# Optimization experiments

Measured on AMD Instinct MI355X. Metric: run time of the kernel, lower is better.

The kernel has to match this reference:

```python
import jax, jax.numpy as jnp
import numpy as np


def _conv3x3(x, w, b):
    # standard 3x3 conv, stride 1, padding 1, NCHW/OIHW
    y = jax.lax.conv_general_dilated(
        x, w, window_strides=(1, 1), padding=((1, 1), (1, 1)),
        dimension_numbers=('NCHW', 'OIHW', 'NCHW'))
    return y + b[None, :, None, None]


def _deform_conv3x3(x, offset, w, b):
    # torchvision-style DeformConv2d: kernel 3x3, stride 1, pad 1, dilation 1,
    # 1 offset group, no mask. offset: [B, 18, H, W] with (dy, dx) per tap.
    B, C, H, W = x.shape
    K = 9
    off = offset.reshape(B, K, 2, H, W)
    ky = (jnp.arange(K) // 3 - 1).astype(x.dtype)[None, :, None, None]
    kx = (jnp.arange(K) % 3 - 1).astype(x.dtype)[None, :, None, None]
    # fractional sample positions per output pixel and kernel tap: [B, K, H, W]
    sy = off[:, :, 0] + ky + jnp.arange(H, dtype=x.dtype)[None, None, :, None]
    sx = off[:, :, 1] + kx + jnp.arange(W, dtype=x.dtype)[None, None, None, :]
    y0f = jnp.floor(sy)
    x0f = jnp.floor(sx)
    dy = sy - y0f
    dx = sx - x0f
    y0 = y0f.astype(jnp.int32)
    x0 = x0f.astype(jnp.int32)

    def sample_b(xb, yi, xi):
        # xb: [C,H,W], yi/xi: [K,H,W] -> [C,K,H,W], zero outside bounds
        valid = (yi >= 0) & (yi < H) & (xi >= 0) & (xi < W)
        yc = jnp.clip(yi, 0, H - 1)
        xc = jnp.clip(xi, 0, W - 1)
        return xb[:, yc, xc] * valid[None].astype(xb.dtype)

    def bilinear_b(xb, y0b, x0b, dyb, dxb):
        v00 = sample_b(xb, y0b, x0b)
        v01 = sample_b(xb, y0b, x0b + 1)
        v10 = sample_b(xb, y0b + 1, x0b)
        v11 = sample_b(xb, y0b + 1, x0b + 1)
        w00 = ((1 - dyb) * (1 - dxb))[None]
        w01 = ((1 - dyb) * dxb)[None]
        w10 = (dyb * (1 - dxb))[None]
        w11 = (dyb * dxb)[None]
        return v00 * w00 + v01 * w01 + v10 * w10 + v11 * w11

    samp = jax.vmap(bilinear_b)(x, y0, x0, dy, dx)  # [B, C, K, H, W]
    Co, Ci = w.shape[0], w.shape[1]
    out = jnp.einsum('oik,bikhw->bohw', w.reshape(Co, Ci, K), samp)
    return out + b[None, :, None, None]


def setup_inputs() -> dict:
    key = jax.random.key(0)
    ks = jax.random.split(key, 5)
    B, C, H, W = 4, 128, 96, 96
    lr = jax.random.normal(ks[0], (B, C, H, W), jnp.float32)
    hr = jax.random.normal(ks[1], (B, C, H, W), jnp.float32)
    w_off = jax.random.normal(ks[2], (18, 2 * C, 3, 3), jnp.float32) * 0.02
    b_off = jnp.zeros((18,), jnp.float32)
    w_def = jax.random.normal(ks[3], (C, C, 3, 3), jnp.float32) / np.float32(np.sqrt(C * 9))
    b_def = jax.random.normal(ks[4], (C,), jnp.float32) * 0.01
    return {"lr_features": lr, "hr_features": hr, "w_off": w_off,
            "b_off": b_off, "w_def": w_def, "b_def": b_def}


def reference(lr_features, hr_features, w_off, b_off, w_def, b_def):
    inp = jnp.concatenate([lr_features, hr_features], axis=1)  # [B, 2C, H, W]
    offset = _conv3x3(inp, w_off, b_off)                        # [B, 18, H, W]
    return _deform_conv3x3(hr_features, offset, w_def, b_def)   # [B, C, H, W]
```

## Files before the change

### kernel.cpp

```cpp
#include <hip/hip_runtime.h>
#include <hip/hip_bf16.h>

#define HH 96
#define WW 96
#define CC 128
#define C2 256
#define PLANE (HH*WW)
#define NGRP 6
#define GP 8
#define NG 16
#define KSG 72
#define ROWS 13
#define NPCHK (ROWS*WW)
#define PCHK_PAD 1280

typedef __attribute__((ext_vector_type(8))) short bf16x8;
typedef __attribute__((ext_vector_type(4))) float f32x4;
typedef __attribute__((ext_vector_type(4))) unsigned int u32x4;

__device__ __forceinline__ int swz(int row, int byte_in_row) {
    return row * 128 + (byte_in_row ^ ((row & 7) << 4));
}

__device__ __forceinline__ void gload_lds16(const void* g, void* l) {
    __builtin_amdgcn_global_load_lds(
        (const __attribute__((address_space(1))) char*)g,
        (__attribute__((address_space(3))) char*)l, 16, 0, 0);
}

__device__ __forceinline__ unsigned pack2(float a, float b) {
    return (unsigned)__bfloat16_as_ushort(__float2bfloat16(a)) |
           ((unsigned)__bfloat16_as_ushort(__float2bfloat16(b)) << 16);
}

#define MFMA16(A,B,C) __builtin_amdgcn_mfma_f32_16x16x32_bf16((A),(B),(C),0,0,0)

#define VMW4() { asm volatile("s_waitcnt vmcnt(4)" ::: "memory"); __builtin_amdgcn_sched_barrier(0); }
#define VMW0() { asm volatile("s_waitcnt vmcnt(0)" ::: "memory"); __builtin_amdgcn_sched_barrier(0); }
#define LGKM0_BAR() { asm volatile("s_waitcnt lgkmcnt(0)" ::: "memory"); \
    __builtin_amdgcn_sched_barrier(0); __builtin_amdgcn_s_barrier(); \
    __builtin_amdgcn_sched_barrier(0); }
#define RAW_BAR() { __builtin_amdgcn_sched_barrier(0); __builtin_amdgcn_s_barrier(); \
    __builtin_amdgcn_sched_barrier(0); }

__global__ __launch_bounds__(256) void prep_kernel(
    const float* __restrict__ hr, const float* __restrict__ lr,
    const float* __restrict__ w_def, const float* __restrict__ w_off,
    unsigned short* __restrict__ hrbf, unsigned short* __restrict__ lrbf,
    unsigned short* __restrict__ wpad, unsigned short* __restrict__ wop)
{
    const int bid = blockIdx.x;
    const int tid = threadIdx.x;
    if (bid < 4608) {
        const bool is_hr = bid < 2304;
        const float* src0 = is_hr ? hr : lr;
        unsigned short* o = is_hr ? hrbf : lrbf;
        int idx = (is_hr ? bid : bid - 2304) * 256 + tid;
        int hw = idx % PLANE;
        int t  = idx / PLANE;
        int g  = t & 15;
        int b  = t >> 4;
        const float* src = src0 + ((size_t)(b * CC + g * GP)) * PLANE + hw;
        unsigned pk[4];
#pragma unroll
        for (int j = 0; j < 4; ++j)
            pk[j] = pack2(src[(size_t)(2*j) * PLANE], src[(size_t)(2*j+1) * PLANE]);
        u32x4 v = {pk[0], pk[1], pk[2], pk[3]};
        *reinterpret_cast<u32x4*>(o + (size_t)idx * 8) = v;
    } else if (bid < 5184) {
        int i = (bid - 4608) * 256 + tid;
        int oc = i / (NG * KSG);
        int r  = i - oc * (NG * KSG);
        int g  = r / KSG;
        int s  = r - g * KSG;
        int tap = s >> 3;
        int icoff = s & 7;
        wpad[i] = __bfloat16_as_ushort(__float2bfloat16(
            w_def[(size_t)(oc * CC + g * GP + icoff) * 9 + tap]));
    } else {
        int i = (bid - 5184) * 256 + tid;
        int oc = i / (32 * KSG);
        int r  = i - oc * (32 * KSG);
        int g  = r / KSG;
        int s  = r - g * KSG;
        int tap = s >> 3;
        int icoff = s & 7;
        int c = g * 8 + icoff;
        float v = (oc < 18) ? w_off[(size_t)(oc * C2 + c) * 9 + tap] : 0.f;
        wop[i] = __bfloat16_as_ushort(__float2bfloat16(v));
    }
}

__global__ __launch_bounds__(256) void wcvt_kernel(const float* __restrict__ w,
                                                   unsigned short* __restrict__ o)
{
    int i = blockIdx.x * 256 + threadIdx.x;
    if (i < CC * NG * KSG) {
        int oc = i / (NG * KSG);
        int r  = i - oc * (NG * KSG);
        int g  = r / KSG;
        int s  = r - g * KSG;
        int tap = s >> 3;
        int icoff = s & 7;
        o[i] = __bfloat16_as_ushort(__float2bfloat16(
            w[(size_t)(oc * CC + g * GP + icoff) * 9 + tap]));
    }
}

__global__ __launch_bounds__(256) void cvt8_kernel(const float* __restrict__ src0,
                                                   unsigned short* __restrict__ o)
{
    int idx = blockIdx.x * 256 + threadIdx.x;
    int hw = idx % PLANE;
    int t  = idx / PLANE;
    int g  = t & 15;
    int b  = t >> 4;
    const float* src = src0 + ((size_t)(b * CC + g * GP)) * PLANE + hw;
    unsigned pk[4];
#pragma unroll
    for (int j = 0; j < 4; ++j)
        pk[j] = pack2(src[(size_t)(2*j) * PLANE], src[(size_t)(2*j+1) * PLANE]);
    u32x4 v = {pk[0], pk[1], pk[2], pk[3]};
    *reinterpret_cast<u32x4*>(o + (size_t)idx * 8) = v;
}

__global__ __launch_bounds__(256) void offset_conv_kernel(
    const float* __restrict__ lr, const float* __restrict__ hr,
    const float* __restrict__ w_off, float* __restrict__ outp)
{
    __shared__ float tile[2][324];
    const int bid = blockIdx.x;
    const int q   = bid % NGRP;
    const int t   = bid / NGRP;
    const int b   = t / 36;
    const int rr  = t % 36;
    const int h0  = (rr / 6) * 16;
    const int w0  = (rr % 6) * 16;
    const int tid = threadIdx.x;
    const int py  = tid >> 4;
    const int px  = tid & 15;

    const int c0 = (C2 * q) / NGRP, c1 = (C2 * (q + 1)) / NGRP;
    const float* srcp = (q < 3) ? lr : hr;
    const int cofs = (q < 3) ? 0 : CC;

    int gy0 = h0 - 1 + tid / 18, gx0 = w0 - 1 + tid % 18;
    bool ok0 = (unsigned)gy0 < (unsigned)HH && (unsigned)gx0 < (unsigned)WW;
    int off0 = gy0 * WW + gx0;
    int j1 = tid + 256;
    int gy1 = h0 - 1 + j1 / 18, gx1 = w0 - 1 + j1 % 18;
    bool ok1 = (j1 < 324) && (unsigned)gy1 < (unsigned)HH && (unsigned)gx1 < (unsigned)WW;
    int off1 = gy1 * WW + gx1;

    float acc[18];
#pragma unroll
    for (int oc = 0; oc < 18; ++oc) acc[oc] = 0.f;

    const float* pl = srcp + (size_t)(b * CC + c0 - cofs) * PLANE;
    float p0 = ok0 ? pl[off0] : 0.f;
    float p1 = ok1 ? pl[off1] : 0.f;

    for (int c = c0; c < c1; ++c) {
        float* tb = tile[c & 1];
        tb[tid] = p0;
        if (j1 < 324) tb[j1] = p1;
        __syncthreads();
        if (c + 1 < c1) {
            const float* pn = srcp + (size_t)(b * CC + c + 1 - cofs) * PLANE;
            p0 = ok0 ? pn[off0] : 0.f;
            p1 = ok1 ? pn[off1] : 0.f;
        }
        float tv[9];
#pragma unroll
        for (int ky = 0; ky < 3; ++ky)
#pragma unroll
            for (int kx = 0; kx < 3; ++kx)
                tv[ky*3+kx] = tb[(py+ky)*18 + px + kx];
#pragma unroll
        for (int oc = 0; oc < 18; ++oc) {
            const float* wp = w_off + (size_t)(oc * C2 + c) * 9;
#pragma unroll
            for (int tap = 0; tap < 9; ++tap)
                acc[oc] = fmaf(wp[tap], tv[tap], acc[oc]);
        }
    }
#pragma unroll
    for (int oc = 0; oc < 18; ++oc)
        outp[((size_t)(b*CC + q*18 + oc)) * PLANE + (h0+py)*WW + (w0+px)] = acc[oc];
}

__global__ __launch_bounds__(768, 6) void offset_mfma_kernel(
    const unsigned short* __restrict__ lrbf, const unsigned short* __restrict__ hrbf,
    const unsigned short* __restrict__ wop, const float* __restrict__ b_off,
    float* __restrict__ offw)
{
    __shared__ __align__(16) unsigned short planes[2][3*WW*8];
    __shared__ __align__(16) unsigned short wgt0[32*64];
    __shared__ __align__(16) unsigned short wgt1[32*8];
    __shared__ __align__(16) unsigned short samp0[2][WW*64];
    __shared__ __align__(16) unsigned short samp1[2][WW*8];

    const int rawb = blockIdx.x;
    const int bid  = (rawb & 7) * 48 + (rawb >> 3);
    const int b    = bid / HH;
    const int h    = bid % HH;
    const int tid  = threadIdx.x;

    const int pri = tid / 96, ppx = tid - (tid / 96) * 96;
    const int prow = min(max(h - 1 + pri, 0), HH - 1);

    const int woc = tid / 9, wsl = tid % 9;
    float4 wv;

#define ISSUE_P(G, PB) { \
    if (tid < 288) { \
        const unsigned short* base_ = ((G) < 16 ? lrbf : hrbf); \
        const unsigned short* src_ = base_ + \
            ((size_t)((b*16 + ((G) & 15))) * PLANE + prow*WW + ppx) * 8; \
        gload_lds16(src_, (char*)planes[PB] + tid*16); \
    } }
#define ISSUE_W(G) { \
    if (tid < 288) \
        wv = *reinterpret_cast<const float4*>(wop + ((size_t)(woc*32 + (G)))*KSG + wsl*8); \
    }
#define WRITE_W() { \
    if (tid < 288) { \
        if (wsl < 8) *reinterpret_cast<float4*>((char*)wgt0 + swz(woc, wsl*16)) = wv; \
        else         *reinterpret_cast<float4*>((char*)wgt1 + woc*16) = wv; \
    } }

    const int tap1 = tid / WW, px1 = tid - (tid / WW) * WW;
    const int ky1 = tap1 / 3 - 1, kx1 = tap1 % 3 - 1;
    const int row1 = h + ky1, x1 = px1 + kx1;
    const bool ok1 = (unsigned)row1 < (unsigned)HH && (unsigned)x1 < (unsigned)WW;
    const int ro1 = ((ky1+1)*WW + x1) * 16;
    const int wr1 = px1*128 + ((tap1*16) ^ ((px1 & 7) << 4));
    const int x2 = tid + 1;
    const bool ok2 = (tid < 96) && (h + 1 < HH) && (x2 < WW);
    const int ro2 = (2*WW + x2) * 16;
    const int wr2 = tid * 16;

    const int lane = tid & 63;
    const int wid  = tid >> 6;
    const int ocg  = wid / 6;
    const int pxg  = wid - ocg * 6;
    const int l15  = lane & 15;
    const int l4   = lane >> 4;
    const int rowA = ocg*16 + l15;
    const int rowB = pxg*16 + l15;
    const bf16x8 zf = {};

    f32x4 acc = (f32x4){0.f, 0.f, 0.f, 0.f};

#define MFMA_O(SB) { \
    bf16x8 a0_ = *reinterpret_cast<const bf16x8*>((char*)wgt0 + swz(rowA, l4*16)); \
    bf16x8 a1_ = *reinterpret_cast<const bf16x8*>((char*)wgt0 + swz(rowA, 64 + l4*16)); \
    bf16x8 a2_ = *reinterpret_cast<const bf16x8*>((char*)wgt1 + rowA*16); \
    if (l4) a2_ = zf; \
    const char* s0_ = (const char*)samp0[SB]; \
    bf16x8 b0_ = *reinterpret_cast<const bf16x8*>(s0_ + swz(rowB, l4*16)); \
    bf16x8 b1_ = *reinterpret_cast<const bf16x8*>(s0_ + swz(rowB, 64 + l4*16)); \
    bf16x8 b2_ = *reinterpret_cast<const bf16x8*>((const char*)samp1[SB] + rowB*16); \
    acc = MFMA16(a0_, b0_, acc); \
    acc = MFMA16(a1_, b1_, acc); \
    acc = MFMA16(a2_, b2_, acc); }

    ISSUE_P(0, 0);
    ISSUE_W(0);

    for (int g2 = 0; g2 < 32; ++g2) {
        const int sb = g2 & 1;
        if (g2) MFMA_O(sb ^ 1);
        __syncthreads();
        WRITE_W();
        {
            u32x4 v = {0u, 0u, 0u, 0u};
            if (ok1) v = *reinterpret_cast<const u32x4*>((const char*)planes[sb] + ro1);
            *reinterpret_cast<u32x4*>((char*)samp0[sb] + wr1) = v;
            if (tid < 96) {
                u32x4 v2 = {0u, 0u, 0u, 0u};
                if (ok2) v2 = *reinterpret_cast<const u32x4*>((const char*)planes[sb] + ro2);
                *reinterpret_cast<u32x4*>((char*)samp1[sb] + wr2) = v2;
            }
        }
        __syncthreads();
        if (g2 < 31) { ISSUE_P(g2 + 1, sb ^ 1); ISSUE_W(g2 + 1); }
    }
    MFMA_O(1);

#pragma unroll
    for (int r = 0; r < 4; ++r) {
        int oc = ocg*16 + l4*4 + r;
        if (oc < 18)
            offw[((size_t)(b*18 + oc)) * PLANE + h*WW + pxg*16 + l15] = acc[r] + b_off[oc];
    }
#undef ISSUE_P
#undef ISSUE_W
#undef WRITE_W
#undef MFMA_O
}

template<bool HRBF, bool OFFWS>
__global__ __launch_bounds__(768, 6) void deform2_kernel(
    const float* __restrict__ hr, const unsigned short* __restrict__ hrbf,
    const float* __restrict__ b_off, const unsigned short* __restrict__ wpad,
    const float* __restrict__ b_def, const float* __restrict__ offw,
    float* __restrict__ outp)
{
    __shared__ __align__(16) unsigned short planes[2][PCHK_PAD*8];
    __shared__ __align__(16) unsigned short wgt0[CC*64];
    __shared__ __align__(16) unsigned short wgt1[CC*8];
    __shared__ __align__(16) unsigned short samp0[WW*64];
    __shared__ __align__(16) unsigned short samp1[WW*8];
    __shared__ __align__(8)  float2 geom[9*97];
    __shared__ float bias_lds[CC];

    const int rawb = blockIdx.x;
    const int bid  = (rawb & 7) * 48 + (rawb >> 3);
    const int b    = bid / HH;
    const int h    = bid % HH;
    const int tid  = threadIdx.x;
    const int r0   = min(max(h - 6, 0), HH - ROWS);

    const float* hrb = hr + (size_t)b * CC * PLANE;

    float4 wv0, wv1;
    const int wc0oc = tid / 9, wc0s = tid % 9;
    const int wt2   = (tid < 384) ? tid + 768 : tid;
    const int wc1oc = wt2 / 9, wc1s = wt2 % 9;
    const int pc2   = (tid < 512) ? tid + 768 : tid;
    const int pcs   = min(pc2, NPCHK - 1);

#define ISSUE_WGT(G) { \
    wv0 = *reinterpret_cast<const float4*>(wpad + ((size_t)(wc0oc*NG + (G))*KSG + wc0s*8)); \
    wv1 = *reinterpret_cast<const float4*>(wpad + ((size_t)(wc1oc*NG + (G))*KSG + wc1s*8)); }
#define WRITE_WGT() { \
    if (wc0s < 8) *reinterpret_cast<float4*>((char*)wgt0 + swz(wc0oc, wc0s*16)) = wv0; \
    else          *reinterpret_cast<float4*>((char*)wgt1 + wc0oc*16) = wv0; \
    if (tid < 384) { \
        if (wc1s < 8) *reinterpret_cast<float4*>((char*)wgt0 + swz(wc1oc, wc1s*16)) = wv1; \
        else          *reinterpret_cast<float4*>((char*)wgt1 + wc1oc*16) = wv1; \
    } }

#define ISSUE_PLANES(G, PB) { \
    const unsigned short* src_ = hrbf + ((size_t)(b*NG + (G))*PLANE + r0*WW)*8; \
    gload_lds16(src_ + (size_t)tid*8, (char*)planes[PB] + tid*16); \
    gload_lds16(src_ + (size_t)pcs*8, (char*)planes[PB] + pc2*16); }

#define STAGE_DIRECT(G, PB) { \
    for (int p = tid; p < NPCHK; p += 768) { \
        int r_ = p / WW, x_ = p - (p / WW) * WW; \
        const float* s_ = hrb + (size_t)((G)*GP) * PLANE + (r0 + r_)*WW + x_; \
        unsigned pk_[4]; \
        _Pragma("unroll") \
        for (int j = 0; j < 4; ++j) \
            pk_[j] = pack2(s_[(size_t)(2*j)*PLANE], s_[(size_t)(2*j+1)*PLANE]); \
        u32x4 v_ = {pk_[0], pk_[1], pk_[2], pk_[3]}; \
        *reinterpret_cast<u32x4*>((char*)planes[PB] + p*16) = v_; \
    } }

    if (HRBF) ISSUE_PLANES(0, 0);
    ISSUE_WGT(0);

    for (int t = tid; t < 9 * WW; t += 768) {
        int tap = t / WW;
        int px  = t - tap * WW;
        int hw  = h * WW + px;
        float offy, offx;
        if (OFFWS) {
            offy = offw[((size_t)(b*18 + 2*tap    )) * PLANE + hw];
            offx = offw[((size_t)(b*18 + 2*tap + 1)) * PLANE + hw];
        } else {
            offy = b_off[2*tap]; offx = b_off[2*tap + 1];
#pragma unroll
            for (int q = 0; q < NGRP; ++q) {
                offy += outp[((size_t)(b*CC + q*18 + 2*tap    )) * PLANE + hw];
                offx += outp[((size_t)(b*CC + q*18 + 2*tap + 1)) * PLANE + hw];
            }
        }
        geom[tap*97 + px] = make_float2((float)h  + (float)(tap/3 - 1) + offy,
                                        (float)px + (float)(tap%3 - 1) + offx);
    }
    if (tid < CC) bias_lds[tid] = b_def[tid];
    if (!HRBF) STAGE_DIRECT(0, 0);
    __syncthreads();

    const int lane = tid & 63;
    const int wid  = tid >> 6;
    const int ocg4 = wid / 3;
    const int pxg  = wid - ocg4 * 3;
    const int l15  = lane & 15;
    const int l4   = lane >> 4;

    f32x4 acc[2][2];
#pragma unroll
    for (int mf = 0; mf < 2; ++mf)
#pragma unroll
        for (int nf = 0; nf < 2; ++nf)
            acc[mf][nf] = (f32x4){0.f, 0.f, 0.f, 0.f};

    const int rowA0 = ocg4*32 + l15, rowA1 = rowA0 + 16;
    const int rowB0 = pxg*32 + l15,  rowB1 = rowB0 + 16;
    const bf16x8 zf = {};

#define MFMA_G() { \
    bf16x8 a00_ = *reinterpret_cast<const bf16x8*>((char*)wgt0 + swz(rowA0, l4*16)); \
    bf16x8 a10_ = *reinterpret_cast<const bf16x8*>((char*)wgt0 + swz(rowA1, l4*16)); \
    bf16x8 a01_ = *reinterpret_cast<const bf16x8*>((char*)wgt0 + swz(rowA0, 64 + l4*16)); \
    bf16x8 a11_ = *reinterpret_cast<const bf16x8*>((char*)wgt0 + swz(rowA1, 64 + l4*16)); \
    bf16x8 a02_ = *reinterpret_cast<const bf16x8*>((char*)wgt1 + rowA0*16); \
    bf16x8 a12_ = *reinterpret_cast<const bf16x8*>((char*)wgt1 + rowA1*16); \
    if (l4) { a02_ = zf; a12_ = zf; } \
    const char* s0_ = (const char*)samp0; \
    const char* s1_ = (const char*)samp1; \
    bf16x8 b00_ = *reinterpret_cast<const bf16x8*>(s0_ + swz(rowB0, l4*16)); \
    bf16x8 b10_ = *reinterpret_cast<const bf16x8*>(s0_ + swz(rowB1, l4*16)); \
    bf16x8 b01_ = *reinterpret_cast<const bf16x8*>(s0_ + swz(rowB0, 64 + l4*16)); \
    bf16x8 b11_ = *reinterpret_cast<const bf16x8*>(s0_ + swz(rowB1, 64 + l4*16)); \
    bf16x8 b02_ = *reinterpret_cast<const bf16x8*>(s1_ + rowB0*16); \
    bf16x8 b12_ = *reinterpret_cast<const bf16x8*>(s1_ + rowB1*16); \
    acc[0][0] = MFMA16(a00_, b00_, acc[0][0]); \
    acc[0][1] = MFMA16(a00_, b10_, acc[0][1]); \
    acc[1][0] = MFMA16(a10_, b00_, acc[1][0]); \
    acc[1][1] = MFMA16(a10_, b10_, acc[1][1]); \
    acc[0][0] = MFMA16(a01_, b01_, acc[0][0]); \
    acc[0][1] = MFMA16(a01_, b11_, acc[0][1]); \
    acc[1][0] = MFMA16(a11_, b01_, acc[1][0]); \
    acc[1][1] = MFMA16(a11_, b11_, acc[1][1]); \
    acc[0][0] = MFMA16(a02_, b02_, acc[0][0]); \
    acc[0][1] = MFMA16(a02_, b12_, acc[0][1]); \
    acc[1][0] = MFMA16(a12_, b02_, acc[1][0]); \
    acc[1][1] = MFMA16(a12_, b12_, acc[1][1]); }

    for (int g = 0; g < NG; ++g) {
        const int pb = g & 1;
        WRITE_WGT();
        if (g < NG - 1) {
            ISSUE_WGT(g + 1);
            if (HRBF) { ISSUE_PLANES(g + 1, pb ^ 1); }
            else      { STAGE_DIRECT(g + 1, pb ^ 1); }
            if (HRBF) { VMW4(); }
        } else {
            if (HRBF) { VMW0(); }
        }
        for (int it = tid; it < 9 * WW; it += 768) {
            int tap = it / WW;
            int px  = it - tap * WW;
            float2 s2 = geom[tap*97 + px];
            float sy = s2.x, sx = s2.y;
            float y0f = floorf(sy), x0f = floorf(sx);
            float dy = sy - y0f, dx = sx - x0f;
            int y0 = (int)y0f, x0 = (int)x0f;
            bool y0v = (unsigned)y0       < (unsigned)HH;
            bool y1v = (unsigned)(y0 + 1) < (unsigned)HH;
            bool x0v = (unsigned)x0       < (unsigned)WW;
            bool x1v = (unsigned)(x0 + 1) < (unsigned)WW;
            float ody = 1.f - dy, odx = 1.f - dx;
            float w00 = (y0v && x0v) ? ody*odx : 0.f;
            float w01 = (y0v && x1v) ? ody*dx  : 0.f;
            float w10 = (y1v && x0v) ? dy*odx  : 0.f;
            float w11 = (y1v && x1v) ? dy*dx   : 0.f;
            int y0c = min(max(y0, 0), HH-1), y1c = min(max(y0+1, 0), HH-1);
            int x0c = min(max(x0, 0), WW-1), x1c = min(max(x0+1, 0), WW-1);
            float sv[GP];
            bool ng = (y0v && (unsigned)(y0 - r0) >= (unsigned)ROWS) ||
                      (y1v && (unsigned)(y1c - r0) >= (unsigned)ROWS);
            if (__builtin_expect(!ng, 1)) {
                int ra = min(max(y0c - r0, 0), ROWS-1);
                int rb = min(max(y1c - r0, 0), ROWS-1);
                const char* pbase = (const char*)planes[pb];
                u32x4 q00 = *reinterpret_cast<const u32x4*>(pbase + (ra*WW + x0c)*16);
                u32x4 q01 = *reinterpret_cast<const u32x4*>(pbase + (ra*WW + x1c)*16);
                u32x4 q10 = *reinterpret_cast<const u32x4*>(pbase + (rb*WW + x0c)*16);
                u32x4 q11 = *reinterpret_cast<const u32x4*>(pbase + (rb*WW + x1c)*16);
#pragma unroll
                for (int j = 0; j < 4; ++j) {
                    float a00 = __uint_as_float(q00[j] << 16), b00 = __uint_as_float(q00[j] & 0xffff0000u);
                    float a01 = __uint_as_float(q01[j] << 16), b01 = __uint_as_float(q01[j] & 0xffff0000u);
                    float a10 = __uint_as_float(q10[j] << 16), b10 = __uint_as_float(q10[j] & 0xffff0000u);
                    float a11 = __uint_as_float(q11[j] << 16), b11 = __uint_as_float(q11[j] & 0xffff0000u);
                    sv[2*j]   = fmaf(w00, a00, fmaf(w01, a01, fmaf(w10, a10, w11*a11)));
                    sv[2*j+1] = fmaf(w00, b00, fmaf(w01, b01, fmaf(w10, b10, w11*b11)));
                }
            } else {
                const float* base = hrb + (size_t)(g*GP) * PLANE;
#pragma unroll
                for (int j = 0; j < GP; ++j) {
                    const float* p = base + (size_t)j * PLANE;
                    sv[j] = fmaf(w00, p[y0c*WW + x0c], fmaf(w01, p[y0c*WW + x1c],
                            fmaf(w10, p[y1c*WW + x0c], w11 * p[y1c*WW + x1c])));
                }
            }
            unsigned pk0 = pack2(sv[0], sv[1]), pk1 = pack2(sv[2], sv[3]);
            unsigned pk2 = pack2(sv[4], sv[5]), pk3 = pack2(sv[6], sv[7]);
            u32x4 pv = {pk0, pk1, pk2, pk3};
            if (tap < 8)
                *reinterpret_cast<u32x4*>((char*)samp0 + swz(px, tap*16)) = pv;
            else
                *reinterpret_cast<u32x4*>((char*)samp1 + px*16) = pv;
        }
        LGKM0_BAR();
        MFMA_G();
        RAW_BAR();
    }

#pragma unroll
    for (int mf = 0; mf < 2; ++mf)
#pragma unroll
        for (int r = 0; r < 4; ++r) {
            int oc = ocg4*32 + mf*16 + l4*4 + r;
            float bd = bias_lds[oc];
#pragma unroll
            for (int nf = 0; nf < 2; ++nf) {
                int px = pxg*32 + nf*16 + l15;
                outp[((size_t)(b*CC + oc)) * PLANE + h*WW + px] = acc[mf][nf][r] + bd;
            }
        }
#undef ISSUE_WGT
#undef WRITE_WGT
#undef ISSUE_PLANES
#undef STAGE_DIRECT
#undef MFMA_G
}

extern "C" void kernel_launch(void* const* d_in, const int* in_sizes, int n_in,
                              void* d_out, int out_size, void* d_ws, size_t ws_size,
                              hipStream_t stream)
{
    const float* lr    = (const float*)d_in[0];
    const float* hr    = (const float*)d_in[1];
    const float* w_off = (const float*)d_in[2];
    const float* b_off = (const float*)d_in[3];
    const float* w_def = (const float*)d_in[4];
    const float* b_def = (const float*)d_in[5];
    float* outp = (float*)d_out;

    const size_t wpad_b = (size_t)CC * NG * KSG * 2 + 256;
    const size_t hrbf_b = (size_t)4 * NG * PLANE * GP * 2;
    const size_t lrbf_b = hrbf_b;
    const size_t woff_b = (size_t)32 * 32 * KSG * 2 + 256;
    const size_t offw_b = (size_t)4 * 18 * PLANE * 4;

    unsigned short* wpad = (unsigned short*)d_ws;
    unsigned short* hrbf = (unsigned short*)((char*)d_ws + wpad_b);
    unsigned short* lrbf = (unsigned short*)((char*)d_ws + wpad_b + hrbf_b);
    unsigned short* wop  = (unsigned short*)((char*)d_ws + wpad_b + hrbf_b + lrbf_b);
    float*          offw = (float*)((char*)d_ws + wpad_b + hrbf_b + lrbf_b + woff_b);

    const bool full     = ws_size >= wpad_b + hrbf_b + lrbf_b + woff_b + offw_b;
    const bool use_hrbf = ws_size >= wpad_b + hrbf_b + lrbf_b;

    if (full) {
        prep_kernel<<<5472, 256, 0, stream>>>(hr, lr, w_def, w_off,
                                              hrbf, lrbf, wpad, wop);
        offset_mfma_kernel<<<4*HH, 768, 0, stream>>>(lrbf, hrbf, wop, b_off, offw);
        deform2_kernel<true, true><<<4*HH, 768, 0, stream>>>(
            hr, hrbf, b_off, wpad, b_def, offw, outp);
    } else {
        wcvt_kernel<<<(CC*NG*KSG + 255)/256, 256, 0, stream>>>(w_def, wpad);
        if (use_hrbf)
            cvt8_kernel<<<(4*NG*PLANE)/256, 256, 0, stream>>>(hr, hrbf);
        offset_conv_kernel<<<4*36*NGRP, 256, 0, stream>>>(lr, hr, w_off, outp);
        if (use_hrbf)
            deform2_kernel<true, false><<<4*HH, 768, 0, stream>>>(
                hr, hrbf, b_off, wpad, b_def, offw, outp);
        else
            deform2_kernel<false, false><<<4*HH, 768, 0, stream>>>(
                hr, hrbf, b_off, wpad, b_def, offw, outp);
    }
}
```

Before: 102.9 us.

## Restructure offset conv pipeline with vmcnt waits and raise MFMA priority

```diff
diff --git a/kernel.cpp b/kernel.cpp
--- a/kernel.cpp
+++ b/kernel.cpp
@@ -36,6 +36,7 @@
 #define MFMA16(A,B,C) __builtin_amdgcn_mfma_f32_16x16x32_bf16((A),(B),(C),0,0,0)
 
 #define VMW4() { asm volatile("s_waitcnt vmcnt(4)" ::: "memory"); __builtin_amdgcn_sched_barrier(0); }
+#define VMW2() { asm volatile("s_waitcnt vmcnt(2)" ::: "memory"); __builtin_amdgcn_sched_barrier(0); }
 #define VMW0() { asm volatile("s_waitcnt vmcnt(0)" ::: "memory"); __builtin_amdgcn_sched_barrier(0); }
 #define LGKM0_BAR() { asm volatile("s_waitcnt lgkmcnt(0)" ::: "memory"); \
     __builtin_amdgcn_sched_barrier(0); __builtin_amdgcn_s_barrier(); \
@@ -197,8 +198,8 @@
     __shared__ __align__(16) unsigned short planes[2][3*WW*8];
     __shared__ __align__(16) unsigned short wgt0[32*64];
     __shared__ __align__(16) unsigned short wgt1[32*8];
-    __shared__ __align__(16) unsigned short samp0[2][WW*64];
-    __shared__ __align__(16) unsigned short samp1[2][WW*8];
+    __shared__ __align__(16) unsigned short samp0[WW*64];
+    __shared__ __align__(16) unsigned short samp1[WW*8];
 
     const int rawb = blockIdx.x;
     const int bid  = (rawb & 7) * 48 + (rawb >> 3);
@@ -252,41 +253,49 @@
 
     f32x4 acc = (f32x4){0.f, 0.f, 0.f, 0.f};
 
-#define MFMA_O(SB) { \
+#define MFMA_O() { \
     bf16x8 a0_ = *reinterpret_cast<const bf16x8*>((char*)wgt0 + swz(rowA, l4*16)); \
     bf16x8 a1_ = *reinterpret_cast<const bf16x8*>((char*)wgt0 + swz(rowA, 64 + l4*16)); \
     bf16x8 a2_ = *reinterpret_cast<const bf16x8*>((char*)wgt1 + rowA*16); \
     if (l4) a2_ = zf; \
-    const char* s0_ = (const char*)samp0[SB]; \
-    bf16x8 b0_ = *reinterpret_cast<const bf16x8*>(s0_ + swz(rowB, l4*16)); \
-    bf16x8 b1_ = *reinterpret_cast<const bf16x8*>(s0_ + swz(rowB, 64 + l4*16)); \
-    bf16x8 b2_ = *reinterpret_cast<const bf16x8*>((const char*)samp1[SB] + rowB*16); \
+    bf16x8 b0_ = *reinterpret_cast<const bf16x8*>((char*)samp0 + swz(rowB, l4*16)); \
+    bf16x8 b1_ = *reinterpret_cast<const bf16x8*>((char*)samp0 + swz(rowB, 64 + l4*16)); \
+    bf16x8 b2_ = *reinterpret_cast<const bf16x8*>((char*)samp1 + rowB*16); \
     acc = MFMA16(a0_, b0_, acc); \
     acc = MFMA16(a1_, b1_, acc); \
     acc = MFMA16(a2_, b2_, acc); }
 
+    ISSUE_W(0);
     ISSUE_P(0, 0);
-    ISSUE_W(0);
+    __syncthreads();
 
     for (int g2 = 0; g2 < 32; ++g2) {
         const int sb = g2 & 1;
-        if (g2) MFMA_O(sb ^ 1);
-        __syncthreads();
         WRITE_W();
+        if (g2 < 31) {
+            ISSUE_W(g2 + 1);
+            ISSUE_P(g2 + 1, sb ^ 1);
+            VMW2();
+        } else {
+            VMW0();
+        }
+        RAW_BAR();
         {
             u32x4 v = {0u, 0u, 0u, 0u};
             if (ok1) v = *reinterpret_cast<const u32x4*>((const char*)planes[sb] + ro1);
-            *reinterpret_cast<u32x4*>((char*)samp0[sb] + wr1) = v;
+            *reinterpret_cast<u32x4*>((char*)samp0 + wr1) = v;
             if (tid < 96) {
                 u32x4 v2 = {0u, 0u, 0u, 0u};
                 if (ok2) v2 = *reinterpret_cast<const u32x4*>((const char*)planes[sb] + ro2);
-                *reinterpret_cast<u32x4*>((char*)samp1[sb] + wr2) = v2;
+                *reinterpret_cast<u32x4*>((char*)samp1 + wr2) = v2;
             }
         }
-        __syncthreads();
-        if (g2 < 31) { ISSUE_P(g2 + 1, sb ^ 1); ISSUE_W(g2 + 1); }
-    }
-    MFMA_O(1);
+        LGKM0_BAR();
+        __builtin_amdgcn_s_setprio(1);
+        MFMA_O();
+        __builtin_amdgcn_s_setprio(0);
+        RAW_BAR();
+    }
 
 #pragma unroll
     for (int r = 0; r < 4; ++r) {
@@ -500,7 +509,9 @@
                 *reinterpret_cast<u32x4*>((char*)samp1 + px*16) = pv;
         }
         LGKM0_BAR();
+        __builtin_amdgcn_s_setprio(1);
         MFMA_G();
+        __builtin_amdgcn_s_setprio(0);
         RAW_BAR();
     }
 
```

After: 99.79 us. 1.03x faster.
